# Kernel optimization log

Measured on AMD Instinct MI355X. Metric: run time of the kernel, lower is better.

## Reference

```python
import jax, jax.numpy as jnp
import numpy as np

HID = 768
INTER = 3072
H = 12
DH = 64
N = 16384
W = 256   # attention_width
L = 512   # per-sequence length (power of 2, used via the uint32 bit-mask trick)


def rotate_every_two(x):
    x1 = x[..., ::2]
    x2 = x[..., 1::2]
    return jnp.stack((-x2, x1), axis=-1).reshape(x.shape)


def setup_inputs() -> dict:
    key = jax.random.key(0)
    ks = jax.random.split(key, 6)
    # GPT-J style interleaved rotary tables: sin/cos each value repeated twice
    inv_freq = 1.0 / (10000.0 ** (np.arange(0, DH, 2) / DH))  # [DH/2]
    ang = np.arange(N)[:, None] * inv_freq[None, :]           # [N, DH/2]
    pos_sin = jnp.asarray(np.repeat(np.sin(ang), 2, axis=-1), dtype=jnp.float32)
    pos_cos = jnp.asarray(np.repeat(np.cos(ang), 2, axis=-1), dtype=jnp.float32)
    return {
        "x": jax.random.normal(ks[0], (N, HID), dtype=jnp.float32),
        "normed_ages": jax.random.normal(ks[1], (N,), dtype=jnp.float32),
        "pos_sin": pos_sin,
        "pos_cos": pos_cos,
        "ln_scale": jnp.ones((HID,), dtype=jnp.float32),
        "ln_offset": jnp.zeros((HID,), dtype=jnp.float32),
        "w_in": jax.random.normal(ks[2], (HID, 3 * HID + INTER), dtype=jnp.float32) * 0.02,
        "b_in": jnp.zeros((3 * HID + INTER,), dtype=jnp.float32),
        "w_out": jax.random.normal(ks[3], (HID + INTER, HID), dtype=jnp.float32) * 0.02,
        "b_out": jnp.zeros((HID,), dtype=jnp.float32),
        "length": L,
    }


def reference(x, normed_ages, pos_sin, pos_cos, ln_scale, ln_offset,
              w_in, b_in, w_out, b_out, length):
    # LayerNorm (haiku: eps=1e-5, create_scale/offset)
    mu = jnp.mean(x, axis=-1, keepdims=True)
    var = jnp.var(x, axis=-1, keepdims=True)
    xn = (x - mu) * jax.lax.rsqrt(var + 1e-5) * ln_scale + ln_offset

    # fused QKV + FF projection (note: original computes x_with_ages but never uses it)
    mid = xn @ w_in + b_in
    q, k, v, ff = jnp.split(mid, [HID, 2 * HID, 3 * HID], axis=-1)

    def to_heads(t):  # [N, HID] -> [H, N, DH]
        return t.reshape(N, H, DH).transpose(1, 0, 2)

    q, k, v = to_heads(q), to_heads(k), to_heads(v)

    # rotary ('per_head'): sincos broadcast over heads
    sin, cos = pos_sin[None], pos_cos[None]
    q = q * cos + rotate_every_two(q) * sin
    k = k * cos + rotate_every_two(k) * sin

    # local (sliding-window, causal, within-sequence) attention, chunked by W
    C = W
    nc = N // C
    qc = q.reshape(H, nc, C, DH)
    kc = k.reshape(H, nc, C, DH)
    vc = v.reshape(H, nc, C, DH)
    kprev = jnp.concatenate([jnp.zeros_like(kc[:, :1]), kc[:, :-1]], axis=1)
    vprev = jnp.concatenate([jnp.zeros_like(vc[:, :1]), vc[:, :-1]], axis=1)
    kcat = jnp.concatenate([kprev, kc], axis=2)  # [H, nc, 2C, DH]
    vcat = jnp.concatenate([vprev, vc], axis=2)

    qi = (jnp.arange(nc) * C)[:, None] + jnp.arange(C)        # [nc, C]
    kj = (jnp.arange(nc) * C)[:, None] - C + jnp.arange(2 * C)  # [nc, 2C]
    lm = ~(jnp.uint32(length) - jnp.uint32(1))  # same bit-trick as the module
    same_seq = ((qi[:, :, None].astype(jnp.uint32) & lm) ==
                (jnp.maximum(kj, 0)[:, None, :].astype(jnp.uint32) & lm))
    d = qi[:, :, None] - kj[:, None, :]
    mask = (kj[:, None, :] >= 0) & (d >= 0) & (d < W) & same_seq  # [nc, C, 2C]

    scale = 1.0 / jnp.sqrt(jnp.float32(DH))
    scores = jnp.einsum('hncd,hnkd->hnck', qc, kcat) * scale
    scores = jnp.where(mask[None], scores, jnp.float32(-1e30))
    probs = jax.nn.softmax(scores, axis=-1)
    attn = jnp.einsum('hnck,hnkd->hncd', probs, vcat)

    attn = attn.reshape(H, N, DH).transpose(1, 0, 2).reshape(N, HID)
    combined = jnp.concatenate([attn, jax.nn.gelu(ff)], axis=-1)
    return xn + combined @ w_out + b_out
```

## Files before the change

kernel.cpp:

```cpp
#include <hip/hip_runtime.h>

#define N_TOK 16384
#define HIDN  768
#define MIDN  5376
#define COMBN 3840
#define NH    12
#define DHD   64
#define CHUNK 256
#define WIN   256

typedef short s16x8 __attribute__((ext_vector_type(8)));
typedef short s16x4 __attribute__((ext_vector_type(4)));
typedef float f32x4 __attribute__((ext_vector_type(4)));

__device__ __forceinline__ float bf2f(unsigned short u){
  union { unsigned u; float f; } x; x.u = ((unsigned)u) << 16; return x.f;
}
__device__ __forceinline__ unsigned short f2bf(float f){
  union { float f; unsigned u; } x; x.f = f;
  unsigned r = x.u + 0x7fffu + ((x.u >> 16) & 1u);
  return (unsigned short)(r >> 16);
}
__device__ __forceinline__ float gelu_tanh(float x){
  float u = 0.7978845608028654f * (x + 0.044715f * x * x * x);
  u = fminf(fmaxf(u, -30.f), 30.f);
  float e = __expf(2.f * u);
  return 0.5f * x * (1.f + (e - 1.f) / (e + 1.f));
}
__device__ __forceinline__ void glds16(const void* g, void* l){
  __builtin_amdgcn_global_load_lds(
      (const __attribute__((address_space(1))) unsigned*)g,
      (__attribute__((address_space(3))) unsigned*)l, 16, 0, 0);
}

__global__ __launch_bounds__(256) void transpose_f2b(
    const float* __restrict__ in, unsigned short* __restrict__ out,
    int R, int Cc)
{
  __shared__ short t[64 * 72];
  const int tid = threadIdx.x;
  const int r0 = blockIdx.y * 64, c0 = blockIdx.x * 64;
  #pragma unroll
  for (int rep = 0; rep < 4; rep++){
    int v = tid + 256 * rep;
    int r = v >> 4, s = v & 15;
    float4 d = *(const float4*)(in + (size_t)(r0 + r) * Cc + c0 + s * 4);
    s16x4 o = { (short)f2bf(d.x), (short)f2bf(d.y), (short)f2bf(d.z), (short)f2bf(d.w) };
    *(s16x4*)(t + r * 72 + s * 4) = o;
  }
  __syncthreads();
  #pragma unroll
  for (int rep = 0; rep < 2; rep++){
    int v = tid + 256 * rep;
    int c = v & 63, s2 = v >> 6;
    s16x8 d;
    #pragma unroll
    for (int j = 0; j < 8; j++) d[j] = t[(s2 * 8 + j) * 72 + c];
    *(s16x8*)(out + (size_t)(c0 + c) * R + r0 + s2 * 8) = d;
  }
}

__global__ __launch_bounds__(256) void ln_kernel(
    const float* __restrict__ x, const float* __restrict__ sc,
    const float* __restrict__ ofs, unsigned short* __restrict__ xn)
{
  const int lane = threadIdx.x & 63, wv = threadIdx.x >> 6;
  const int row = blockIdx.x * 4 + wv;
  const float4* xr = (const float4*)(x + (size_t)row * HIDN);
  float4 vals[3];
  float sum = 0.f, sq = 0.f;
  #pragma unroll
  for (int j = 0; j < 3; j++){
    vals[j] = xr[lane + 64 * j];
    sum += vals[j].x + vals[j].y + vals[j].z + vals[j].w;
    sq  += vals[j].x * vals[j].x + vals[j].y * vals[j].y
         + vals[j].z * vals[j].z + vals[j].w * vals[j].w;
  }
  #pragma unroll
  for (int o = 1; o < 64; o <<= 1){ sum += __shfl_xor(sum, o); sq += __shfl_xor(sq, o); }
  const float mu = sum * (1.f / HIDN);
  const float rs = rsqrtf(fmaxf(sq * (1.f / HIDN) - mu * mu, 0.f) + 1e-5f);
  s16x4* xo = (s16x4*)(xn + (size_t)row * HIDN);
  const float4* scp = (const float4*)sc;
  const float4* ofp = (const float4*)ofs;
  #pragma unroll
  for (int j = 0; j < 3; j++){
    int p = lane + 64 * j;
    float4 s = scp[p], o = ofp[p];
    s16x4 w;
    w[0] = (short)f2bf((vals[j].x - mu) * rs * s.x + o.x);
    w[1] = (short)f2bf((vals[j].y - mu) * rs * s.y + o.y);
    w[2] = (short)f2bf((vals[j].z - mu) * rs * s.z + o.z);
    w[3] = (short)f2bf((vals[j].w - mu) * rs * s.w + o.w);
    xo[p] = w;
  }
}

__global__ __launch_bounds__(256) void gemm_bt(
    const unsigned short* __restrict__ A, const unsigned short* __restrict__ BT,
    const float* __restrict__ bias, int K, int mode,
    unsigned short* __restrict__ qb, unsigned short* __restrict__ kb,
    unsigned short* __restrict__ vb, unsigned short* __restrict__ comb,
    const unsigned short* __restrict__ xn, float* __restrict__ outp)
{
  __shared__ short As[128 * 32];
  __shared__ short Bs[128 * 32];
  const int tid = threadIdx.x, lane = tid & 63, wv = tid >> 6;
  const int quad = lane >> 4, l15 = lane & 15;
  const int m0 = blockIdx.y * 128, n0 = blockIdx.x * 128;
  const int wr = (wv >> 1) * 64, wc = (wv & 1) * 64;

  f32x4 acc[4][4];
  #pragma unroll
  for (int i = 0; i < 4; i++)
    #pragma unroll
    for (int j = 0; j < 4; j++) acc[i][j] = (f32x4){0.f,0.f,0.f,0.f};

  const int srow = tid >> 2, sseg = tid & 3;
  const unsigned short* Ap = A  + (size_t)(m0 + srow) * K + sseg * 8;
  const unsigned short* Bp = BT + (size_t)(n0 + srow) * K + sseg * 8;
  const size_t rstep = (size_t)64 * K;
  char* AsB = ((char*)As) + tid * 16;
  char* BsB = ((char*)Bs) + tid * 16;

  for (int kt = 0; kt < K; kt += 32){
    __syncthreads();
    glds16(Ap + kt,         AsB);
    glds16(Ap + kt + rstep, AsB + 4096);
    glds16(Bp + kt,         BsB);
    glds16(Bp + kt + rstep, BsB + 4096);
    __syncthreads();
    s16x8 a[4], b[4];
    #pragma unroll
    for (int rt = 0; rt < 4; rt++) a[rt] = *(const s16x8*)(As + (wr + rt*16 + l15)*32 + quad*8);
    #pragma unroll
    for (int ct = 0; ct < 4; ct++) b[ct] = *(const s16x8*)(Bs + (wc + ct*16 + l15)*32 + quad*8);
    #pragma unroll
    for (int rt = 0; rt < 4; rt++)
      #pragma unroll
      for (int ct = 0; ct < 4; ct++)
        acc[rt][ct] = __builtin_amdgcn_mfma_f32_16x16x32_bf16(a[rt], b[ct], acc[rt][ct], 0, 0, 0);
  }

  #pragma unroll
  for (int rt = 0; rt < 4; rt++){
    #pragma unroll
    for (int ct = 0; ct < 4; ct++){
      const int col = n0 + wc + ct * 16 + l15;
      const float bsv = bias[col];
      #pragma unroll
      for (int r = 0; r < 4; r++){
        const int row = m0 + wr + rt * 16 + quad * 4 + r;
        float val = acc[rt][ct][r] + bsv;
        if (mode == 0){
          if (col < 2304){
            unsigned short* dst; int cc;
            if (col < 768)      { dst = qb; cc = col; }
            else if (col < 1536){ dst = kb; cc = col - 768; }
            else                { dst = vb; cc = col - 1536; }
            dst[((size_t)(cc >> 6) * N_TOK + row) * DHD + (cc & 63)] = f2bf(val);
          } else {
            comb[(size_t)row * COMBN + (col - 1536)] = f2bf(gelu_tanh(val));
          }
        } else {
          const size_t o = (size_t)row * HIDN + col;
          outp[o] = bf2f(xn[o]) + val;
        }
      }
    }
  }
}

__global__ __launch_bounds__(256) void rope_qk(
    unsigned short* __restrict__ qb, unsigned short* __restrict__ kb,
    const float* __restrict__ psin, const float* __restrict__ pcos)
{
  __shared__ float ss[2048], cc[2048];
  const int tid = threadIdx.x, g = blockIdx.x;
  #pragma unroll
  for (int rep = 0; rep < 8; rep++){
    int idx = rep * 256 + tid;
    int tok = idx >> 5, p = idx & 31;
    size_t gt = ((size_t)(g * 64 + tok)) * DHD + 2 * p;
    ss[idx] = psin[gt];
    cc[idx] = pcos[gt];
  }
  __syncthreads();
  unsigned* q32 = (unsigned*)qb;
  unsigned* k32 = (unsigned*)kb;
  for (int h = 0; h < NH; h++){
    #pragma unroll
    for (int rep = 0; rep < 8; rep++){
      int idx = rep * 256 + tid;
      int tok = idx >> 5, p = idx & 31;
      size_t a = ((size_t)h * N_TOK + g * 64 + tok) * 32 + p;
      float s = ss[tok * 32 + p], c0 = cc[tok * 32 + p];
      unsigned u = q32[a];
      float e = bf2f((unsigned short)(u & 0xffff));
      float d = bf2f((unsigned short)(u >> 16));
      q32[a] = (unsigned)f2bf((e * c0 - d * s) * 0.125f)
             | (((unsigned)f2bf((d * c0 + e * s) * 0.125f)) << 16);
      u = k32[a];
      e = bf2f((unsigned short)(u & 0xffff));
      d = bf2f((unsigned short)(u >> 16));
      k32[a] = (unsigned)f2bf(e * c0 - d * s)
             | (((unsigned)f2bf(d * c0 + e * s)) << 16);
    }
  }
}

__global__ __launch_bounds__(256) void attn_kernel(
    const unsigned short* __restrict__ qb, const unsigned short* __restrict__ kb,
    const unsigned short* __restrict__ vb, unsigned short* __restrict__ comb,
    const int* __restrict__ lenp)
{
  __shared__ short Ks[2][64 * 72];
  __shared__ short Vt[2][64 * 64];
  __shared__ short Ps[4][16 * 72];
  const int tid = threadIdx.x, lane = tid & 63, wv = tid >> 6;
  const int quad = lane >> 4, l15 = lane & 15;
  const int h = blockIdx.y, c = blockIdx.x;
  const unsigned lm = ~((unsigned)lenp[0] - 1u);
  const int i0 = c * CHUNK + wv * 64;
  const unsigned short* qh = qb + (size_t)h * N_TOK * DHD;
  const unsigned short* kh = kb + (size_t)h * N_TOK * DHD;
  const unsigned short* vh = vb + (size_t)h * N_TOK * DHD;

  s16x8 qf[4][2];
  #pragma unroll
  for (int rt = 0; rt < 4; rt++){
    const unsigned short* qr = qh + (size_t)(i0 + rt * 16 + l15) * DHD;
    qf[rt][0] = *(const s16x8*)(qr + quad * 8);
    qf[rt][1] = *(const s16x8*)(qr + 32 + quad * 8);
  }

  f32x4 O[4][4];
  float mm[4][4], ll[4][4];
  #pragma unroll
  for (int rt = 0; rt < 4; rt++)
    #pragma unroll
    for (int j = 0; j < 4; j++){ O[rt][j] = (f32x4){0,0,0,0}; mm[rt][j] = -1e30f; ll[rt][j] = 0.f; }
  short* myP = &Ps[wv][0];

  const int skey = tid & 63, sseg = tid >> 6;
  const int jb0 = c * CHUNK - 256;
  s16x8 kr[2], vr[2];

  auto issue = [&](int jb){
    if (jb >= 0){
      const unsigned short* kp = kh + (size_t)(jb + skey) * DHD + sseg * 16;
      const unsigned short* vp = vh + (size_t)(jb + skey) * DHD + sseg * 16;
      kr[0] = *(const s16x8*)(kp);     kr[1] = *(const s16x8*)(kp + 8);
      vr[0] = *(const s16x8*)(vp);     vr[1] = *(const s16x8*)(vp + 8);
    } else {
      kr[0] = kr[1] = vr[0] = vr[1] = (s16x8){0,0,0,0,0,0,0,0};
    }
  };

  issue(jb0);
  for (int tb = 0; tb < 8; tb++){
    const int jb = jb0 + tb * 64;
    const int buf = tb & 1;
    short* Kb = &Ks[buf][0];
    short* Vb = &Vt[buf][0];
    *(s16x8*)(Kb + skey * 72 + sseg * 16)     = kr[0];
    *(s16x8*)(Kb + skey * 72 + sseg * 16 + 8) = kr[1];
    #pragma unroll
    for (int half = 0; half < 2; half++)
      #pragma unroll
      for (int j = 0; j < 8; j++){
        const int d = sseg * 16 + half * 8 + j;
        Vb[d * 64 + (((skey & 56) ^ ((d & 7) << 3)) | (skey & 7))] = vr[half][j];
      }
    if (tb < 7) issue(jb + 64);
    __syncthreads();

    const bool act = (jb >= 0) && (jb <= i0 + 63) && (jb + 63 >= i0 - 255) &&
                     (((unsigned)i0 & lm) == ((unsigned)jb & lm));
    if (!act) continue;

    #pragma unroll
    for (int rt = 0; rt < 4; rt++){
      const int ilo = i0 + rt * 16;
      if (ilo + 15 < jb || ilo - (jb + 63) >= WIN) continue;
      f32x4 sc[4];
      #pragma unroll
      for (int ct = 0; ct < 4; ct++){
        const short* kbase = Kb + (ct * 16 + l15) * 72 + quad * 8;
        const s16x8 b0 = *(const s16x8*)(kbase);
        const s16x8 b1 = *(const s16x8*)(kbase + 32);
        f32x4 a = (f32x4){0,0,0,0};
        a = __builtin_amdgcn_mfma_f32_16x16x32_bf16(qf[rt][0], b0, a, 0, 0, 0);
        a = __builtin_amdgcn_mfma_f32_16x16x32_bf16(qf[rt][1], b1, a, 0, 0, 0);
        sc[ct] = a;
      }
      float alph[4];
      #pragma unroll
      for (int r = 0; r < 4; r++){
        const int i = ilo + quad * 4 + r;
        #pragma unroll
        for (int ct = 0; ct < 4; ct++){
          const unsigned dd = (unsigned)(i - (jb + ct * 16 + l15));
          if (dd >= 256u) sc[ct][r] = -1e30f;
        }
        float mx = fmaxf(fmaxf(sc[0][r], sc[1][r]), fmaxf(sc[2][r], sc[3][r]));
        mx = fmaxf(mx, __shfl_xor(mx, 1));
        mx = fmaxf(mx, __shfl_xor(mx, 2));
        mx = fmaxf(mx, __shfl_xor(mx, 4));
        mx = fmaxf(mx, __shfl_xor(mx, 8));
        const float mnew = fmaxf(mm[rt][r], mx);
        alph[r] = __expf(mm[rt][r] - mnew);
        mm[rt][r] = mnew;
        float p0 = __expf(sc[0][r] - mnew);
        float p1 = __expf(sc[1][r] - mnew);
        float p2 = __expf(sc[2][r] - mnew);
        float p3 = __expf(sc[3][r] - mnew);
        sc[0][r] = p0; sc[1][r] = p1; sc[2][r] = p2; sc[3][r] = p3;
        float rsum = (p0 + p1) + (p2 + p3);
        rsum += __shfl_xor(rsum, 1);
        rsum += __shfl_xor(rsum, 2);
        rsum += __shfl_xor(rsum, 4);
        rsum += __shfl_xor(rsum, 8);
        ll[rt][r] = ll[rt][r] * alph[r] + rsum;
      }
      #pragma unroll
      for (int co = 0; co < 4; co++)
        #pragma unroll
        for (int r = 0; r < 4; r++) O[rt][co][r] *= alph[r];
      #pragma unroll
      for (int r = 0; r < 4; r++){
        const int prow = quad * 4 + r;
        #pragma unroll
        for (int ct = 0; ct < 4; ct++)
          myP[prow * 72 + ct * 16 + l15] = (short)f2bf(sc[ct][r]);
      }
      #pragma unroll
      for (int ks2 = 0; ks2 < 2; ks2++){
        const s16x8 pf = *(const s16x8*)(myP + l15 * 72 + ks2 * 32 + quad * 8);
        #pragma unroll
        for (int co = 0; co < 4; co++){
          const int d = co * 16 + l15;
          const s16x8 vf = *(const s16x8*)(Vb + d * 64 +
                              ((ks2 * 32 + quad * 8) ^ ((d & 7) << 3)));
          O[rt][co] = __builtin_amdgcn_mfma_f32_16x16x32_bf16(pf, vf, O[rt][co], 0, 0, 0);
        }
      }
    }
  }

  #pragma unroll
  for (int rt = 0; rt < 4; rt++)
    #pragma unroll
    for (int co = 0; co < 4; co++)
      #pragma unroll
      for (int r = 0; r < 4; r++){
        const int tok = i0 + rt * 16 + quad * 4 + r;
        comb[(size_t)tok * COMBN + h * DHD + co * 16 + l15] = f2bf(O[rt][co][r] / ll[rt][r]);
      }
}

extern "C" void kernel_launch(void* const* d_in, const int* in_sizes, int n_in,
                              void* d_out, int out_size, void* d_ws, size_t ws_size,
                              hipStream_t stream)
{
  const float* x     = (const float*)d_in[0];
  const float* psin  = (const float*)d_in[2];
  const float* pcos  = (const float*)d_in[3];
  const float* lns   = (const float*)d_in[4];
  const float* lno   = (const float*)d_in[5];
  const float* w_in  = (const float*)d_in[6];
  const float* b_in  = (const float*)d_in[7];
  const float* w_out = (const float*)d_in[8];
  const float* b_out = (const float*)d_in[9];
  const int*   lenp  = (const int*)d_in[10];
  float* out = (float*)d_out;

  char* ws = (char*)d_ws;
  size_t off = 0;
  unsigned short* xn    = (unsigned short*)(ws + off); off += (size_t)N_TOK * HIDN * 2;
  unsigned short* wInT  = (unsigned short*)(ws + off); off += (size_t)MIDN * HIDN * 2;
  unsigned short* wOutT = (unsigned short*)(ws + off); off += (size_t)HIDN * COMBN * 2;
  unsigned short* qbuf  = (unsigned short*)(ws + off); off += (size_t)NH * N_TOK * DHD * 2;
  unsigned short* kbuf  = (unsigned short*)(ws + off); off += (size_t)NH * N_TOK * DHD * 2;
  unsigned short* vbuf  = (unsigned short*)(ws + off); off += (size_t)NH * N_TOK * DHD * 2;
  unsigned short* comb  = (unsigned short*)(ws + off); off += (size_t)N_TOK * COMBN * 2;

  transpose_f2b<<<dim3(MIDN/64, HIDN/64), 256, 0, stream>>>(w_in, wInT, HIDN, MIDN);
  transpose_f2b<<<dim3(HIDN/64, COMBN/64), 256, 0, stream>>>(w_out, wOutT, COMBN, HIDN);
  ln_kernel<<<dim3(N_TOK/4), 256, 0, stream>>>(x, lns, lno, xn);
  gemm_bt<<<dim3(MIDN/128, N_TOK/128), 256, 0, stream>>>(
      xn, wInT, b_in, HIDN, 0, qbuf, kbuf, vbuf, comb, nullptr, nullptr);
  rope_qk<<<dim3(N_TOK/64), 256, 0, stream>>>(qbuf, kbuf, psin, pcos);
  attn_kernel<<<dim3(N_TOK/CHUNK, NH), 256, 0, stream>>>(
      qbuf, kbuf, vbuf, comb, lenp);
  gemm_bt<<<dim3(HIDN/128, N_TOK/128), 256, 0, stream>>>(
      comb, wOutT, b_out, COMBN, 1, nullptr, nullptr, nullptr, nullptr, xn, out);
}
```

Before: 723.7 us.

## Specialize GEMMs, swizzle LDS, use token-major QKV layout, larger GEMM1 tile

The shared GEMM is split into two specialized kernels. The first projection now uses a 256x128 tile with launch bounds allowing two blocks, and the GEMM1 epilogue is simplified. Both GEMMs use an XOR swizzle on the LDS layout to reduce bank conflicts. Q/K/V are now stored token-major ([N, HID]) rather than head-major, which gives contiguous epilogue writes; rope and attention are changed to index this layout. GELU is rewritten in the x*sigmoid form, which is algebraically the same tanh approximation but cheaper; the larger tile risks register pressure, and attention loads of K/V now stride across tokens.

```diff
diff --git a/kernel.cpp b/kernel.cpp
--- a/kernel.cpp
+++ b/kernel.cpp
@@ -21,11 +21,9 @@
   unsigned r = x.u + 0x7fffu + ((x.u >> 16) & 1u);
   return (unsigned short)(r >> 16);
 }
-__device__ __forceinline__ float gelu_tanh(float x){
-  float u = 0.7978845608028654f * (x + 0.044715f * x * x * x);
-  u = fminf(fmaxf(u, -30.f), 30.f);
-  float e = __expf(2.f * u);
-  return 0.5f * x * (1.f + (e - 1.f) / (e + 1.f));
+__device__ __forceinline__ float gelu_fast(float x){
+  float u = -1.5957691216057308f * (x + 0.044715f * x * x * x);
+  return x / (1.f + __expf(u));
 }
 __device__ __forceinline__ void glds16(const void* g, void* l){
   __builtin_amdgcn_global_load_lds(
@@ -96,13 +94,94 @@
   }
 }
 
-__global__ __launch_bounds__(256) void gemm_bt(
+__device__ __forceinline__ int swz(int row, int quad){
+  return row * 64 + ((quad ^ ((row >> 1) & 3)) << 4);
+}
+
+__global__ __launch_bounds__(256, 2) void gemm1_k(
     const unsigned short* __restrict__ A, const unsigned short* __restrict__ BT,
-    const float* __restrict__ bias, int K, int mode,
+    const float* __restrict__ bias,
     unsigned short* __restrict__ qb, unsigned short* __restrict__ kb,
-    unsigned short* __restrict__ vb, unsigned short* __restrict__ comb,
-    const unsigned short* __restrict__ xn, float* __restrict__ outp)
-{
+    unsigned short* __restrict__ vb, unsigned short* __restrict__ comb)
+{
+  constexpr int K = HIDN;
+  __shared__ short As[256 * 32];
+  __shared__ short Bs[128 * 32];
+  const int tid = threadIdx.x, lane = tid & 63, wv = tid >> 6;
+  const int quad = lane >> 4, l15 = lane & 15;
+  const int n0 = blockIdx.x * 128, m0 = blockIdx.y * 256;
+
+  f32x4 acc[4][8];
+  #pragma unroll
+  for (int i = 0; i < 4; i++)
+    #pragma unroll
+    for (int j = 0; j < 8; j++) acc[i][j] = (f32x4){0.f,0.f,0.f,0.f};
+
+  const int srow = tid >> 2;
+  const int sseg = (tid & 3) ^ ((tid >> 3) & 3);
+  const unsigned short* Ap = A  + (size_t)(m0 + srow) * K + sseg * 8;
+  const unsigned short* Bp = BT + (size_t)(n0 + srow) * K + sseg * 8;
+  const size_t rstep = (size_t)64 * K;
+  char* AsB = ((char*)As) + tid * 16;
+  char* BsB = ((char*)Bs) + tid * 16;
+
+  int offA[4], offB[8];
+  #pragma unroll
+  for (int rt = 0; rt < 4; rt++) offA[rt] = swz(wv * 64 + rt * 16 + l15, quad);
+  #pragma unroll
+  for (int ct = 0; ct < 8; ct++) offB[ct] = swz(ct * 16 + l15, quad);
+
+  for (int kt = 0; kt < K; kt += 32){
+    __syncthreads();
+    glds16(Ap + kt,             AsB);
+    glds16(Ap + kt + rstep,     AsB + 4096);
+    glds16(Ap + kt + 2 * rstep, AsB + 8192);
+    glds16(Ap + kt + 3 * rstep, AsB + 12288);
+    glds16(Bp + kt,             BsB);
+    glds16(Bp + kt + rstep,     BsB + 4096);
+    __syncthreads();
+    s16x8 a[4], b[8];
+    #pragma unroll
+    for (int rt = 0; rt < 4; rt++) a[rt] = *(const s16x8*)((const char*)As + offA[rt]);
+    #pragma unroll
+    for (int ct = 0; ct < 8; ct++) b[ct] = *(const s16x8*)((const char*)Bs + offB[ct]);
+    #pragma unroll
+    for (int rt = 0; rt < 4; rt++)
+      #pragma unroll
+      for (int ct = 0; ct < 8; ct++)
+        acc[rt][ct] = __builtin_amdgcn_mfma_f32_16x16x32_bf16(a[rt], b[ct], acc[rt][ct], 0, 0, 0);
+  }
+
+  unsigned short* dstb; int cb; bool isff = false;
+  if (n0 < 768)       { dstb = qb;   cb = n0; }
+  else if (n0 < 1536) { dstb = kb;   cb = n0 - 768; }
+  else if (n0 < 2304) { dstb = vb;   cb = n0 - 1536; }
+  else                { dstb = comb; cb = n0 - 1536; isff = true; }
+  const int rowstride = isff ? COMBN : HIDN;
+
+  #pragma unroll
+  for (int ct = 0; ct < 8; ct++){
+    const float bsv = bias[n0 + ct * 16 + l15];
+    const int col = cb + ct * 16 + l15;
+    #pragma unroll
+    for (int rt = 0; rt < 4; rt++){
+      #pragma unroll
+      for (int r = 0; r < 4; r++){
+        const int row = m0 + wv * 64 + rt * 16 + quad * 4 + r;
+        float val = acc[rt][ct][r] + bsv;
+        if (isff) val = gelu_fast(val);
+        dstb[(size_t)row * rowstride + col] = f2bf(val);
+      }
+    }
+  }
+}
+
+__global__ __launch_bounds__(256) void gemm2_k(
+    const unsigned short* __restrict__ A, const unsigned short* __restrict__ BT,
+    const float* __restrict__ bias, const unsigned short* __restrict__ xn,
+    float* __restrict__ outp)
+{
+  constexpr int K = COMBN;
   __shared__ short As[128 * 32];
   __shared__ short Bs[128 * 32];
   const int tid = threadIdx.x, lane = tid & 63, wv = tid >> 6;
@@ -116,12 +195,19 @@
     #pragma unroll
     for (int j = 0; j < 4; j++) acc[i][j] = (f32x4){0.f,0.f,0.f,0.f};
 
-  const int srow = tid >> 2, sseg = tid & 3;
+  const int srow = tid >> 2;
+  const int sseg = (tid & 3) ^ ((tid >> 3) & 3);
   const unsigned short* Ap = A  + (size_t)(m0 + srow) * K + sseg * 8;
   const unsigned short* Bp = BT + (size_t)(n0 + srow) * K + sseg * 8;
   const size_t rstep = (size_t)64 * K;
   char* AsB = ((char*)As) + tid * 16;
   char* BsB = ((char*)Bs) + tid * 16;
+
+  int offA[4], offB[4];
+  #pragma unroll
+  for (int rt = 0; rt < 4; rt++) offA[rt] = swz(wr + rt * 16 + l15, quad);
+  #pragma unroll
+  for (int ct = 0; ct < 4; ct++) offB[ct] = swz(wc + ct * 16 + l15, quad);
 
   for (int kt = 0; kt < K; kt += 32){
     __syncthreads();
@@ -132,9 +218,9 @@
     __syncthreads();
     s16x8 a[4], b[4];
     #pragma unroll
-    for (int rt = 0; rt < 4; rt++) a[rt] = *(const s16x8*)(As + (wr + rt*16 + l15)*32 + quad*8);
-    #pragma unroll
-    for (int ct = 0; ct < 4; ct++) b[ct] = *(const s16x8*)(Bs + (wc + ct*16 + l15)*32 + quad*8);
+    for (int rt = 0; rt < 4; rt++) a[rt] = *(const s16x8*)((const char*)As + offA[rt]);
+    #pragma unroll
+    for (int ct = 0; ct < 4; ct++) b[ct] = *(const s16x8*)((const char*)Bs + offB[ct]);
     #pragma unroll
     for (int rt = 0; rt < 4; rt++)
       #pragma unroll
@@ -143,69 +229,54 @@
   }
 
   #pragma unroll
-  for (int rt = 0; rt < 4; rt++){
-    #pragma unroll
-    for (int ct = 0; ct < 4; ct++){
-      const int col = n0 + wc + ct * 16 + l15;
-      const float bsv = bias[col];
+  for (int ct = 0; ct < 4; ct++){
+    const int col = n0 + wc + ct * 16 + l15;
+    const float bsv = bias[col];
+    #pragma unroll
+    for (int rt = 0; rt < 4; rt++){
       #pragma unroll
       for (int r = 0; r < 4; r++){
         const int row = m0 + wr + rt * 16 + quad * 4 + r;
-        float val = acc[rt][ct][r] + bsv;
-        if (mode == 0){
-          if (col < 2304){
-            unsigned short* dst; int cc;
-            if (col < 768)      { dst = qb; cc = col; }
-            else if (col < 1536){ dst = kb; cc = col - 768; }
-            else                { dst = vb; cc = col - 1536; }
-            dst[((size_t)(cc >> 6) * N_TOK + row) * DHD + (cc & 63)] = f2bf(val);
-          } else {
-            comb[(size_t)row * COMBN + (col - 1536)] = f2bf(gelu_tanh(val));
-          }
-        } else {
-          const size_t o = (size_t)row * HIDN + col;
-          outp[o] = bf2f(xn[o]) + val;
-        }
+        const size_t o = (size_t)row * HIDN + col;
+        outp[o] = bf2f(xn[o]) + acc[rt][ct][r] + bsv;
       }
     }
   }
 }
 
-__global__ __launch_bounds__(256) void rope_qk(
+__global__ __launch_bounds__(384) void rope_qk(
     unsigned short* __restrict__ qb, unsigned short* __restrict__ kb,
     const float* __restrict__ psin, const float* __restrict__ pcos)
 {
-  __shared__ float ss[2048], cc[2048];
+  __shared__ float ss[2048], cs[2048];
   const int tid = threadIdx.x, g = blockIdx.x;
   #pragma unroll
-  for (int rep = 0; rep < 8; rep++){
-    int idx = rep * 256 + tid;
-    int tok = idx >> 5, p = idx & 31;
-    size_t gt = ((size_t)(g * 64 + tok)) * DHD + 2 * p;
-    ss[idx] = psin[gt];
-    cc[idx] = pcos[gt];
+  for (int rep = 0; rep < 6; rep++){
+    int idx = rep * 384 + tid;
+    if (idx < 2048){
+      int tok = idx >> 5, p = idx & 31;
+      size_t gt = ((size_t)(g * 64 + tok)) * DHD + 2 * p;
+      ss[idx] = psin[gt];
+      cs[idx] = pcos[gt];
+    }
   }
   __syncthreads();
+  const int p = tid & 31;
   unsigned* q32 = (unsigned*)qb;
   unsigned* k32 = (unsigned*)kb;
-  for (int h = 0; h < NH; h++){
-    #pragma unroll
-    for (int rep = 0; rep < 8; rep++){
-      int idx = rep * 256 + tid;
-      int tok = idx >> 5, p = idx & 31;
-      size_t a = ((size_t)h * N_TOK + g * 64 + tok) * 32 + p;
-      float s = ss[tok * 32 + p], c0 = cc[tok * 32 + p];
-      unsigned u = q32[a];
-      float e = bf2f((unsigned short)(u & 0xffff));
-      float d = bf2f((unsigned short)(u >> 16));
-      q32[a] = (unsigned)f2bf((e * c0 - d * s) * 0.125f)
-             | (((unsigned)f2bf((d * c0 + e * s) * 0.125f)) << 16);
-      u = k32[a];
-      e = bf2f((unsigned short)(u & 0xffff));
-      d = bf2f((unsigned short)(u >> 16));
-      k32[a] = (unsigned)f2bf(e * c0 - d * s)
-             | (((unsigned)f2bf(d * c0 + e * s)) << 16);
-    }
+  for (int tok = 0; tok < 64; tok++){
+    const size_t a = ((size_t)(g * 64 + tok)) * 384 + tid;
+    const float s = ss[tok * 32 + p], c0 = cs[tok * 32 + p];
+    unsigned u = q32[a];
+    float e = bf2f((unsigned short)(u & 0xffff));
+    float d = bf2f((unsigned short)(u >> 16));
+    q32[a] = (unsigned)f2bf((e * c0 - d * s) * 0.125f)
+           | (((unsigned)f2bf((d * c0 + e * s) * 0.125f)) << 16);
+    u = k32[a];
+    e = bf2f((unsigned short)(u & 0xffff));
+    d = bf2f((unsigned short)(u >> 16));
+    k32[a] = (unsigned)f2bf(e * c0 - d * s)
+           | (((unsigned)f2bf(d * c0 + e * s)) << 16);
   }
 }
 
@@ -222,14 +293,14 @@
   const int h = blockIdx.y, c = blockIdx.x;
   const unsigned lm = ~((unsigned)lenp[0] - 1u);
   const int i0 = c * CHUNK + wv * 64;
-  const unsigned short* qh = qb + (size_t)h * N_TOK * DHD;
-  const unsigned short* kh = kb + (size_t)h * N_TOK * DHD;
-  const unsigned short* vh = vb + (size_t)h * N_TOK * DHD;
+  const unsigned short* qh = qb + h * DHD;
+  const unsigned short* kh = kb + h * DHD;
+  const unsigned short* vh = vb + h * DHD;
 
   s16x8 qf[4][2];
   #pragma unroll
   for (int rt = 0; rt < 4; rt++){
-    const unsigned short* qr = qh + (size_t)(i0 + rt * 16 + l15) * DHD;
+    const unsigned short* qr = qh + (size_t)(i0 + rt * 16 + l15) * HIDN;
     qf[rt][0] = *(const s16x8*)(qr + quad * 8);
     qf[rt][1] = *(const s16x8*)(qr + 32 + quad * 8);
   }
@@ -248,8 +319,8 @@
 
   auto issue = [&](int jb){
     if (jb >= 0){
-      const unsigned short* kp = kh + (size_t)(jb + skey) * DHD + sseg * 16;
-      const unsigned short* vp = vh + (size_t)(jb + skey) * DHD + sseg * 16;
+      const unsigned short* kp = kh + (size_t)(jb + skey) * HIDN + sseg * 16;
+      const unsigned short* vp = vh + (size_t)(jb + skey) * HIDN + sseg * 16;
       kr[0] = *(const s16x8*)(kp);     kr[1] = *(const s16x8*)(kp + 8);
       vr[0] = *(const s16x8*)(vp);     vr[1] = *(const s16x8*)(vp + 8);
     } else {
@@ -380,19 +451,19 @@
   unsigned short* xn    = (unsigned short*)(ws + off); off += (size_t)N_TOK * HIDN * 2;
   unsigned short* wInT  = (unsigned short*)(ws + off); off += (size_t)MIDN * HIDN * 2;
   unsigned short* wOutT = (unsigned short*)(ws + off); off += (size_t)HIDN * COMBN * 2;
-  unsigned short* qbuf  = (unsigned short*)(ws + off); off += (size_t)NH * N_TOK * DHD * 2;
-  unsigned short* kbuf  = (unsigned short*)(ws + off); off += (size_t)NH * N_TOK * DHD * 2;
-  unsigned short* vbuf  = (unsigned short*)(ws + off); off += (size_t)NH * N_TOK * DHD * 2;
+  unsigned short* qbuf  = (unsigned short*)(ws + off); off += (size_t)N_TOK * HIDN * 2;
+  unsigned short* kbuf  = (unsigned short*)(ws + off); off += (size_t)N_TOK * HIDN * 2;
+  unsigned short* vbuf  = (unsigned short*)(ws + off); off += (size_t)N_TOK * HIDN * 2;
   unsigned short* comb  = (unsigned short*)(ws + off); off += (size_t)N_TOK * COMBN * 2;
 
   transpose_f2b<<<dim3(MIDN/64, HIDN/64), 256, 0, stream>>>(w_in, wInT, HIDN, MIDN);
   transpose_f2b<<<dim3(HIDN/64, COMBN/64), 256, 0, stream>>>(w_out, wOutT, COMBN, HIDN);
   ln_kernel<<<dim3(N_TOK/4), 256, 0, stream>>>(x, lns, lno, xn);
-  gemm_bt<<<dim3(MIDN/128, N_TOK/128), 256, 0, stream>>>(
-      xn, wInT, b_in, HIDN, 0, qbuf, kbuf, vbuf, comb, nullptr, nullptr);
-  rope_qk<<<dim3(N_TOK/64), 256, 0, stream>>>(qbuf, kbuf, psin, pcos);
+  gemm1_k<<<dim3(MIDN/128, N_TOK/256), 256, 0, stream>>>(
+      xn, wInT, b_in, qbuf, kbuf, vbuf, comb);
+  rope_qk<<<dim3(N_TOK/64), 384, 0, stream>>>(qbuf, kbuf, psin, pcos);
   attn_kernel<<<dim3(N_TOK/CHUNK, NH), 256, 0, stream>>>(
       qbuf, kbuf, vbuf, comb, lenp);
-  gemm_bt<<<dim3(HIDN/128, N_TOK/128), 256, 0, stream>>>(
-      comb, wOutT, b_out, COMBN, 1, nullptr, nullptr, nullptr, nullptr, xn, out);
-}
+  gemm2_k<<<dim3(HIDN/128, N_TOK/128), 256, 0, stream>>>(
+      comb, wOutT, b_out, xn, out);
+}
```

Result: faster. 692.6 us (-4.3%).
